# Kernel tuning notes

Measured on AMD Instinct MI355X. Metric: run time of the kernel, lower is better.

Reference implementation:

```python
import jax, jax.numpy as jnp
import numpy as np

N = 100000   # nodes
E = 1600000  # edges (avg degree 16)
D = 128      # in = hid = out dim
EPS = 1e-5   # BatchNorm eps


def setup_inputs() -> dict:
    key = jax.random.key(0)
    ks = jax.random.split(key, 14)
    x = jax.random.normal(ks[0], (N, D), dtype=jnp.float32)
    row = jax.random.randint(ks[1], (E,), 0, N, dtype=jnp.int32)
    col = jax.random.randint(ks[2], (E,), 0, N, dtype=jnp.int32)
    edge_weight = jax.random.uniform(ks[3], (E,), dtype=jnp.float32)
    s = 1.0 / np.sqrt(D)
    W0 = jax.random.uniform(ks[4], (D, D), jnp.float32, -s, s)
    b0 = jax.random.uniform(ks[5], (D,), jnp.float32, -s, s)
    W1 = jax.random.uniform(ks[6], (D, D), jnp.float32, -s, s)
    b1 = jax.random.uniform(ks[7], (D,), jnp.float32, -s, s)
    W2 = jax.random.uniform(ks[8], (D, D), jnp.float32, -s, s)
    b2 = jax.random.uniform(ks[9], (D,), jnp.float32, -s, s)
    g0 = jnp.ones((D,), jnp.float32); be0 = jnp.zeros((D,), jnp.float32)
    g1 = jnp.ones((D,), jnp.float32); be1 = jnp.zeros((D,), jnp.float32)
    return {"x": x, "edge_weight": edge_weight,
            "W0": W0, "b0": b0, "g0": g0, "be0": be0,
            "W1": W1, "b1": b1, "g1": g1, "be1": be1,
            "W2": W2, "b2": b2, "row": row, "col": col}


def _spmm(edge_weight, row, col, h):
    # (A_norm @ h) with A in COO: out[r] = sum_e w_e * h[col_e] for row_e == r
    return jax.ops.segment_sum(edge_weight[:, None] * h[col], row, num_segments=N)


def _bn(h, gamma, beta):
    # BatchNorm1d, training-mode stats (biased variance), over the node axis
    m = h.mean(axis=0)
    v = h.var(axis=0)
    return gamma * (h - m) * jax.lax.rsqrt(v + EPS) + beta


def reference(x, edge_weight, W0, b0, g0, be0, W1, b1, g1, be1, W2, b2, row, col):
    # hidden block 1: SpMM(A, Linear(h)) -> BN -> ReLU (dropout p=0)
    h = jax.nn.relu(_bn(_spmm(edge_weight, row, col, x @ W0 + b0), g0, be0))
    # hidden block 2
    h = jax.nn.relu(_bn(_spmm(edge_weight, row, col, h @ W1 + b1), g1, be1))
    # final layer: SpMM(A, Linear(h)), no BN/activation
    return _spmm(edge_weight, row, col, h @ W2 + b2)
```

## Files before the change

### kernel.cpp

```cpp
#include <hip/hip_runtime.h>
#include <cstddef>

#define DD 128
#define EPS 1e-5f

typedef short short8 __attribute__((ext_vector_type(8)));
typedef float float4v __attribute__((ext_vector_type(4)));

__device__ __forceinline__ unsigned short f2bf(float f) {
    union { float f; unsigned int u; } x; x.f = f;
    unsigned int r = x.u + 0x7fffu + ((x.u >> 16) & 1u);
    return (unsigned short)(r >> 16);
}
__device__ __forceinline__ float bfhi2f(unsigned int hi_bits) {
    union { unsigned int u; float f; } x; x.u = hi_bits;
    return x.f;
}


__global__ void hist_kernel(const int* __restrict__ row, int* __restrict__ deg, int E) {
    int e = blockIdx.x * blockDim.x + threadIdx.x;
    if (e < E) atomicAdd(&deg[row[e]], 1);
}

__global__ void scanA_kernel(const int* __restrict__ deg, int* __restrict__ tmp,
                             int* __restrict__ bsum, int n) {
    __shared__ int s[1024];
    int tid = threadIdx.x;
    int gid = blockIdx.x * 1024 + tid;
    int v = (gid < n) ? ((deg[gid] + 3) & ~3) : 0;
    s[tid] = v;
    __syncthreads();
    for (int off = 1; off < 1024; off <<= 1) {
        int t = s[tid];
        int u = (tid >= off) ? s[tid - off] : 0;
        __syncthreads();
        s[tid] = t + u;
        __syncthreads();
    }
    if (gid < n) tmp[gid] = s[tid];
    if (tid == 1023) bsum[blockIdx.x] = s[1023];
}

__global__ void scanB_kernel(const int* __restrict__ bsum, int* __restrict__ boff,
                             int* __restrict__ row_start, int nb, int n) {
    __shared__ int s[128];
    int tid = threadIdx.x;
    int v = (tid < nb) ? bsum[tid] : 0;
    s[tid] = v;
    __syncthreads();
    for (int off = 1; off < 128; off <<= 1) {
        int t = s[tid];
        int u = (tid >= off) ? s[tid - off] : 0;
        __syncthreads();
        s[tid] = t + u;
        __syncthreads();
    }
    if (tid < nb) boff[tid] = s[tid] - v;
    if (tid == nb - 1) row_start[n] = s[tid];
}

__global__ void scanC_kernel(const int* __restrict__ deg, const int* __restrict__ tmp,
                             const int* __restrict__ boff, int* __restrict__ row_start,
                             int* __restrict__ cursor, int n) {
    int gid = blockIdx.x * 1024 + threadIdx.x;
    if (gid < n) {
        int pd = (deg[gid] + 3) & ~3;
        int rs = tmp[gid] - pd + boff[blockIdx.x];
        row_start[gid] = rs;
        cursor[gid] = rs;
    }
}


__global__ void bcur_init_kernel(const int* __restrict__ row_start,
                                 int* __restrict__ bcur, int nb) {
    int b = blockIdx.x * 256 + threadIdx.x;
    if (b < nb) bcur[b] = row_start[b << 8];
}

__global__ __launch_bounds__(256) void scatter_phase1_kernel(
    const int* __restrict__ row, const int* __restrict__ col,
    const float* __restrict__ ew, int* __restrict__ bcur,
    unsigned long long* __restrict__ ebuf2, int E, int nbuck) {
    __shared__ int hist[512];
    __shared__ int cur[512];
    int tid = threadIdx.x;
    int b = blockIdx.x;
    int C = (E + gridDim.x - 1) / gridDim.x;
    int e0 = b * C, e1 = min(E, e0 + C);
    for (int t = tid; t < nbuck; t += 256) hist[t] = 0;
    __syncthreads();
    for (int e = e0 + tid; e < e1; e += 256)
        atomicAdd(&hist[row[e] >> 8], 1);
    __syncthreads();
    for (int i = tid; i < nbuck; i += 256) {
        int t = i + b * 37;
        t -= (t >= nbuck) ? nbuck * (t / nbuck) : 0;
        int h = hist[t];
        cur[t] = h ? atomicAdd(&bcur[t], h) : 0;
    }
    __syncthreads();
    for (int e = e0 + tid; e < e1; e += 256) {
        int r = row[e];
        int bk = r >> 8;
        int pos = atomicAdd(&cur[bk], 1);
        unsigned long long pk = (unsigned long long)((unsigned int)col[e]
                              | ((unsigned int)(r & 255) << 24))
                              | ((unsigned long long)__float_as_uint(ew[e]) << 32);
        ebuf2[pos] = pk;
    }
}

#define P2CAP 6144

__global__ __launch_bounds__(256) void scatter_phase2_kernel(
    const unsigned long long* __restrict__ ebuf2, const int* __restrict__ row_start,
    const int* __restrict__ bcur_final, int* __restrict__ cursor,
    unsigned long long* __restrict__ ebuf, int N) {
    __shared__ int cur[256];
    __shared__ unsigned long long outb[P2CAP];
    int b = blockIdx.x;
    int r_lo = b << 8;
    int r_hi = min(N, r_lo + 256);
    int e_lo = row_start[r_lo];
    int e_hi = row_start[r_hi];
    int cnt_pad = e_hi - e_lo;
    int cnt_real = bcur_final[b] - e_lo;
    int tid = threadIdx.x;
    if (cnt_pad <= P2CAP) {
        int r = r_lo + tid;
        cur[tid] = (r < N) ? (row_start[r] - e_lo) : 0;
        for (int i = tid; i < cnt_pad; i += 256) outb[i] = 0ull;
        __syncthreads();
        for (int i = e_lo + tid; i < e_lo + cnt_real; i += 256) {
            unsigned long long pk = ebuf2[i];
            int rl = (int)((unsigned int)(pk >> 24) & 255u);
            int pos = atomicAdd(&cur[rl], 1);
            outb[pos] = pk & 0xFFFFFFFF0001FFFFull;
        }
        __syncthreads();
        for (int i = tid; i < cnt_pad; i += 256)
            ebuf[e_lo + i] = outb[i];
    } else {
        for (int i = e_lo + tid; i < e_hi; i += 256) ebuf[i] = 0ull;
        __threadfence();
        __syncthreads();
        for (int i = e_lo + tid; i < e_lo + cnt_real; i += 256) {
            unsigned long long pk = ebuf2[i];
            int rl = (int)((unsigned int)(pk >> 24) & 255u);
            int pos = atomicAdd(&cursor[r_lo + rl], 1);
            ebuf[pos] = pk & 0xFFFFFFFF0001FFFFull;
        }
    }
}


__global__ void convw_kernel(const float* __restrict__ W0, const float* __restrict__ W1,
                             const float* __restrict__ W2, unsigned short* __restrict__ T0,
                             unsigned short* __restrict__ T1, unsigned short* __restrict__ T2) {
    const float* W = (blockIdx.y == 0) ? W0 : (blockIdx.y == 1) ? W1 : W2;
    unsigned short* T = (blockIdx.y == 0) ? T0 : (blockIdx.y == 1) ? T1 : T2;
    int gid = blockIdx.x * 256 + threadIdx.x;
    int k = gid >> 7, n = gid & 127;
    T[n * DD + k] = f2bf(W[k * DD + n]);
}


__global__ __launch_bounds__(256) void gemm_mfma_f32_kernel(
    const float* __restrict__ A, const unsigned short* __restrict__ Wt,
    const float* __restrict__ bias, unsigned short* __restrict__ H, int nrows)
{
    __shared__ unsigned short Asl[64][136];
    __shared__ unsigned short Wsl[128][136];

    const int tid  = threadIdx.x;
    const int row0 = blockIdx.x * 64;

    for (int i = tid; i < 2048; i += 256) {
        int r = i >> 4, off = (i & 15) * 8;
        *(uint4*)&Wsl[r][off] = *(const uint4*)(Wt + (size_t)r * DD + off);
    }
    for (int i = tid; i < 2048; i += 256) {
        int r = i >> 5, off4 = i & 31;
        int grow = row0 + r;
        float4 v = make_float4(0.f, 0.f, 0.f, 0.f);
        if (grow < nrows)
            v = *(const float4*)(A + (size_t)grow * DD + off4 * 4);
        ushort4 p;
        p.x = f2bf(v.x); p.y = f2bf(v.y); p.z = f2bf(v.z); p.w = f2bf(v.w);
        *(ushort4*)&Asl[r][off4 * 4] = p;
    }
    __syncthreads();

    const int w = tid >> 6, lane = tid & 63;
    const int m = lane & 15, q = lane >> 4;

    short8 afr[4];
    #pragma unroll
    for (int c = 0; c < 4; ++c)
        afr[c] = *(const short8*)&Asl[w * 16 + m][c * 32 + q * 8];

    float4v acc[8];
    #pragma unroll
    for (int t = 0; t < 8; ++t) acc[t] = (float4v){0.f, 0.f, 0.f, 0.f};

    #pragma unroll
    for (int t = 0; t < 8; ++t) {
        #pragma unroll
        for (int c = 0; c < 4; ++c) {
            short8 bfr = *(const short8*)&Wsl[t * 16 + m][c * 32 + q * 8];
            acc[t] = __builtin_amdgcn_mfma_f32_16x16x32_bf16(afr[c], bfr, acc[t], 0, 0, 0);
        }
    }

    #pragma unroll
    for (int t = 0; t < 8; ++t) {
        float bv = bias[t * 16 + m];
        #pragma unroll
        for (int i = 0; i < 4; ++i)
            Asl[w * 16 + q * 4 + i][t * 16 + m] = f2bf(acc[t][i] + bv);
    }
    __syncthreads();

    for (int i = tid; i < 1024; i += 256) {
        int r = i >> 4, off = (i & 15) * 8;
        if (row0 + r < nrows)
            *(uint4*)(H + (size_t)(row0 + r) * DD + off) = *(const uint4*)&Asl[r][off];
    }
}


__global__ __launch_bounds__(256) void gemm_mfma_bf16_kernel(
    const unsigned int* __restrict__ A, const unsigned short* __restrict__ Wt,
    const float* __restrict__ bias,
    const float* __restrict__ sums, const float* __restrict__ g,
    const float* __restrict__ be,
    unsigned short* __restrict__ H, int nrows)
{
    __shared__ unsigned short Asl[64][136];
    __shared__ unsigned short Wsl[128][136];
    __shared__ float scl_s[128], sft_s[128];

    const int tid  = threadIdx.x;
    const int row0 = blockIdx.x * 64;

    if (tid < 128) {
        float inv_n = 1.0f / (float)nrows;
        float mean = sums[tid] * inv_n;
        float var = sums[128 + tid] * inv_n - mean * mean;
        float rstd = rsqrtf(var + EPS);
        float sc = g[tid] * rstd;
        scl_s[tid] = sc;
        sft_s[tid] = be[tid] - mean * sc;
    }

    for (int i = tid; i < 2048; i += 256) {
        int r = i >> 4, off = (i & 15) * 8;
        *(uint4*)&Wsl[r][off] = *(const uint4*)(Wt + (size_t)r * DD + off);
    }
    __syncthreads();

    for (int i = tid; i < 1024; i += 256) {
        int r = i >> 4, ch = (i & 15) * 8;
        int grow = row0 + r;
        uint4 u = make_uint4(0, 0, 0, 0);
        if (grow < nrows)
            u = *(const uint4*)(A + (size_t)grow * 64 + (ch >> 1));
        unsigned int uu[4] = {u.x, u.y, u.z, u.w};
        unsigned int outp[4];
        #pragma unroll
        for (int j = 0; j < 4; ++j) {
            float vx = bfhi2f(uu[j] << 16);
            float vy = bfhi2f(uu[j] & 0xffff0000u);
            int k = ch + j * 2;
            vx = fmaxf(0.f, vx * scl_s[k] + sft_s[k]);
            vy = fmaxf(0.f, vy * scl_s[k + 1] + sft_s[k + 1]);
            outp[j] = (unsigned int)f2bf(vx) | ((unsigned int)f2bf(vy) << 16);
        }
        *(uint4*)&Asl[r][ch] = *(const uint4*)outp;
    }
    __syncthreads();

    const int w = tid >> 6, lane = tid & 63;
    const int m = lane & 15, q = lane >> 4;

    short8 afr[4];
    #pragma unroll
    for (int c = 0; c < 4; ++c)
        afr[c] = *(const short8*)&Asl[w * 16 + m][c * 32 + q * 8];

    float4v acc[8];
    #pragma unroll
    for (int t = 0; t < 8; ++t) acc[t] = (float4v){0.f, 0.f, 0.f, 0.f};

    #pragma unroll
    for (int t = 0; t < 8; ++t) {
        #pragma unroll
        for (int c = 0; c < 4; ++c) {
            short8 bfr = *(const short8*)&Wsl[t * 16 + m][c * 32 + q * 8];
            acc[t] = __builtin_amdgcn_mfma_f32_16x16x32_bf16(afr[c], bfr, acc[t], 0, 0, 0);
        }
    }

    #pragma unroll
    for (int t = 0; t < 8; ++t) {
        float bv = bias[t * 16 + m];
        #pragma unroll
        for (int i = 0; i < 4; ++i)
            Asl[w * 16 + q * 4 + i][t * 16 + m] = f2bf(acc[t][i] + bv);
    }
    __syncthreads();

    for (int i = tid; i < 1024; i += 256) {
        int r = i >> 4, off = (i & 15) * 8;
        if (row0 + r < nrows)
            *(uint4*)(H + (size_t)(row0 + r) * DD + off) = *(const uint4*)&Asl[r][off];
    }
}


__global__ __launch_bounds__(256, 8) void spmm_bf16_kernel(
    const unsigned short* __restrict__ H, const int* __restrict__ ps,
    const unsigned long long* __restrict__ ebuf,
    float* __restrict__ Sf, unsigned int* __restrict__ Sb, int writeBF,
    int N, int K)
{
    const int lane = threadIdx.x & 63;
    const int g = lane >> 4;
    const int p = lane & 15;
    const int wave = (blockIdx.x << 2) | (threadIdx.x >> 6);
    int r0 = wave * K;
    if (r0 >= N) return;
    int r1 = min(N, r0 + K);

    const unsigned short* Hp = H + p * 8;

    int r = r0;
    int e = ps[r0];
    const int eEnd = ps[r1];

    while (r < r1 && ps[r + 1] == e) {
        if (g == 0) {
            if (writeBF) {
                uint4 z = make_uint4(0, 0, 0, 0);
                *(uint4*)(Sb + (size_t)r * 64 + p * 4) = z;
            } else {
                float4 z = make_float4(0.f, 0.f, 0.f, 0.f);
                *(float4*)(Sf + (size_t)r * DD + p * 8) = z;
                *(float4*)(Sf + (size_t)r * DD + p * 8 + 4) = z;
            }
        }
        ++r;
    }
    if (r >= r1) return;
    int next_end = ps[r + 1];

    unsigned long long pk_cur = __builtin_nontemporal_load(&ebuf[e + g]);
    int i1 = e + 4; i1 = (i1 < eEnd) ? i1 : e;
    unsigned long long pk_nxt = __builtin_nontemporal_load(&ebuf[i1 + g]);
    uint4 u_cur = *(const uint4*)(Hp + (size_t)(unsigned int)pk_cur * DD);

    float acc[8];
    #pragma unroll
    for (int j = 0; j < 8; ++j) acc[j] = 0.f;

    for (; e < eEnd; e += 4) {
        int i2 = e + 8; i2 = (i2 < eEnd) ? i2 : e;
        unsigned long long pk_f = __builtin_nontemporal_load(&ebuf[i2 + g]);
        uint4 u_nxt = *(const uint4*)(Hp + (size_t)(unsigned int)pk_nxt * DD);
        float wj = __uint_as_float((unsigned int)(pk_cur >> 32));
        unsigned int uu[4] = {u_cur.x, u_cur.y, u_cur.z, u_cur.w};
        #pragma unroll
        for (int q4 = 0; q4 < 4; ++q4) {
            acc[2 * q4]     += wj * bfhi2f(uu[q4] << 16);
            acc[2 * q4 + 1] += wj * bfhi2f(uu[q4] & 0xffff0000u);
        }

        while (e + 4 == next_end) {
            #pragma unroll
            for (int j = 0; j < 8; ++j) {
                acc[j] += __shfl_xor(acc[j], 16);
                acc[j] += __shfl_xor(acc[j], 32);
            }
            if (g == 0) {
                if (writeBF) {
                    unsigned int o[4];
                    #pragma unroll
                    for (int j = 0; j < 4; ++j)
                        o[j] = (unsigned int)f2bf(acc[2 * j])
                             | ((unsigned int)f2bf(acc[2 * j + 1]) << 16);
                    *(uint4*)(Sb + (size_t)r * 64 + p * 4) = *(const uint4*)o;
                } else {
                    float4 lo = make_float4(acc[0], acc[1], acc[2], acc[3]);
                    float4 hi = make_float4(acc[4], acc[5], acc[6], acc[7]);
                    *(float4*)(Sf + (size_t)r * DD + p * 8) = lo;
                    *(float4*)(Sf + (size_t)r * DD + p * 8 + 4) = hi;
                }
            }
            #pragma unroll
            for (int j = 0; j < 8; ++j) acc[j] = 0.f;
            ++r;
            if (r >= r1) break;
            next_end = ps[r + 1];
        }

        pk_cur = pk_nxt;
        u_cur  = u_nxt;
        pk_nxt = pk_f;
    }
}


__global__ void bn_stats_bf16_kernel(const unsigned int* __restrict__ Sb,
                                     float* __restrict__ sums, int n) {
    __shared__ float lsx[256], lsx2[256], lsy[256], lsy2[256];
    int tid = threadIdx.x;
    int c2 = tid & 63;
    float sx = 0.f, sx2 = 0.f, sy = 0.f, sy2 = 0.f;
    int total = n * 64;
    for (int i = blockIdx.x * 256 + tid; i < total; i += 256 * 256) {
        unsigned int u = Sb[i];
        float vx = bfhi2f(u << 16);
        float vy = bfhi2f(u & 0xffff0000u);
        sx += vx; sx2 += vx * vx;
        sy += vy; sy2 += vy * vy;
    }
    lsx[tid] = sx; lsx2[tid] = sx2; lsy[tid] = sy; lsy2[tid] = sy2;
    __syncthreads();
    if (tid < 64) {
        sx  = lsx[tid]  + lsx[tid + 64]  + lsx[tid + 128]  + lsx[tid + 192];
        sx2 = lsx2[tid] + lsx2[tid + 64] + lsx2[tid + 128] + lsx2[tid + 192];
        sy  = lsy[tid]  + lsy[tid + 64]  + lsy[tid + 128]  + lsy[tid + 192];
        sy2 = lsy2[tid] + lsy2[tid + 64] + lsy2[tid + 128] + lsy2[tid + 192];
        atomicAdd(&sums[2 * c2], sx);
        atomicAdd(&sums[2 * c2 + 1], sy);
        atomicAdd(&sums[128 + 2 * c2], sx2);
        atomicAdd(&sums[129 + 2 * c2], sy2);
    }
}


extern "C" void kernel_launch(void* const* d_in, const int* in_sizes, int n_in,
                              void* d_out, int out_size, void* d_ws, size_t ws_size,
                              hipStream_t stream) {
    const float* x   = (const float*)d_in[0];
    const float* ew  = (const float*)d_in[1];
    const float* W0  = (const float*)d_in[2];
    const float* b0  = (const float*)d_in[3];
    const float* g0  = (const float*)d_in[4];
    const float* be0 = (const float*)d_in[5];
    const float* W1  = (const float*)d_in[6];
    const float* b1  = (const float*)d_in[7];
    const float* g1  = (const float*)d_in[8];
    const float* be1 = (const float*)d_in[9];
    const float* W2  = (const float*)d_in[10];
    const float* b2  = (const float*)d_in[11];
    const int* row   = (const int*)d_in[12];
    const int* col   = (const int*)d_in[13];

    const int N = in_sizes[0] / DD;
    const int E = in_sizes[1];
    float* out = (float*)d_out;

    const size_t EPADCAP = (size_t)E + 3 * (size_t)N + 64;

    char* w = (char*)d_ws;
    unsigned short* H   = (unsigned short*)w; w += (size_t)N * DD * 2;
    unsigned int* Sb    = (unsigned int*)w;   w += (size_t)N * 64 * 4;
    unsigned long long* ebuf = (unsigned long long*)w; w += EPADCAP * 8;
    unsigned short* Wt0 = (unsigned short*)w; w += DD * DD * 2;
    unsigned short* Wt1 = (unsigned short*)w; w += DD * DD * 2;
    unsigned short* Wt2 = (unsigned short*)w; w += DD * DD * 2;
    float* sums         = (float*)w;          w += 256 * 4;
    int*   deg          = (int*)w;            w += (size_t)N * 4;
    int*   tmp          = (int*)w;            w += (size_t)N * 4;
    int*   cursor       = (int*)w;            w += (size_t)N * 4;
    int*   bsum         = (int*)w;            w += 128 * 4;
    int*   boff         = (int*)w;            w += 128 * 4;
    int*   row_start    = (int*)w;            w += (size_t)(N + 1) * 4;

    unsigned long long* ebuf2 = (unsigned long long*)Sb;
    int* bcur = tmp;
    int nbuck = (N + 255) >> 8;

    hipMemsetAsync(deg, 0, (size_t)N * 4, stream);
    hist_kernel<<<(E + 255) / 256, 256, 0, stream>>>(row, deg, E);
    int NB = (N + 1023) / 1024;
    scanA_kernel<<<NB, 1024, 0, stream>>>(deg, tmp, bsum, N);
    scanB_kernel<<<1, 128, 0, stream>>>(bsum, boff, row_start, NB, N);
    scanC_kernel<<<NB, 1024, 0, stream>>>(deg, tmp, boff, row_start, cursor, N);
    bcur_init_kernel<<<(nbuck + 255) / 256, 256, 0, stream>>>(row_start, bcur, nbuck);
    scatter_phase1_kernel<<<256, 256, 0, stream>>>(row, col, ew, bcur, ebuf2, E, nbuck);
    scatter_phase2_kernel<<<nbuck, 256, 0, stream>>>(ebuf2, row_start, bcur, cursor, ebuf, N);

    convw_kernel<<<dim3(64, 3), 256, 0, stream>>>(W0, W1, W2, Wt0, Wt1, Wt2);

    int gblocks = (N + 63) / 64;

    const int SPMM_BLOCKS = 2048;
    const int totalWaves = SPMM_BLOCKS * 4;
    const int K = (N + totalWaves - 1) / totalWaves;

    gemm_mfma_f32_kernel<<<gblocks, 256, 0, stream>>>(x, Wt0, b0, H, N);
    spmm_bf16_kernel<<<SPMM_BLOCKS, 256, 0, stream>>>(H, row_start, ebuf, nullptr, Sb, 1, N, K);
    hipMemsetAsync(sums, 0, 256 * 4, stream);
    bn_stats_bf16_kernel<<<256, 256, 0, stream>>>(Sb, sums, N);

    gemm_mfma_bf16_kernel<<<gblocks, 256, 0, stream>>>(Sb, Wt1, b1, sums, g0, be0, H, N);
    spmm_bf16_kernel<<<SPMM_BLOCKS, 256, 0, stream>>>(H, row_start, ebuf, nullptr, Sb, 1, N, K);
    hipMemsetAsync(sums, 0, 256 * 4, stream);
    bn_stats_bf16_kernel<<<256, 256, 0, stream>>>(Sb, sums, N);

    gemm_mfma_bf16_kernel<<<gblocks, 256, 0, stream>>>(Sb, Wt2, b2, sums, g1, be1, H, N);
    spmm_bf16_kernel<<<SPMM_BLOCKS, 256, 0, stream>>>(H, row_start, ebuf, out, nullptr, 0, N, K);
}
```

Baseline: 583.6 us.

## Fuse BN statistics into SpMM epilogue and load GEMM A-fragments directly from global

The separate BN-stats kernel is removed. Each SpMM wave now accumulates per-channel sums and squared sums of the bf16 outputs it writes and reduces them per block into a partial buffer, and a small reduce kernel atomically combines those partials. This avoids re-reading the full hidden activation from memory twice per forward pass. The GEMM kernels skip staging A in LDS and load and convert their MFMA A-fragments straight from global memory. The bcur init kernel is folded into scanC, and the SpMM grid is doubled to 4096 blocks. The trade-offs are added LDS, syncthreads and registers in the SpMM kernel, and a new partial buffer of SPMM_BLOCKS*256 floats in the workspace.

```diff
diff --git a/kernel.cpp b/kernel.cpp
--- a/kernel.cpp
+++ b/kernel.cpp
@@ -62,22 +62,17 @@
 
 __global__ void scanC_kernel(const int* __restrict__ deg, const int* __restrict__ tmp,
                              const int* __restrict__ boff, int* __restrict__ row_start,
-                             int* __restrict__ cursor, int n) {
+                             int* __restrict__ cursor, int* __restrict__ bcur, int n) {
     int gid = blockIdx.x * 1024 + threadIdx.x;
     if (gid < n) {
         int pd = (deg[gid] + 3) & ~3;
         int rs = tmp[gid] - pd + boff[blockIdx.x];
         row_start[gid] = rs;
         cursor[gid] = rs;
-    }
-}
-
-
-__global__ void bcur_init_kernel(const int* __restrict__ row_start,
-                                 int* __restrict__ bcur, int nb) {
-    int b = blockIdx.x * 256 + threadIdx.x;
-    if (b < nb) bcur[b] = row_start[b << 8];
-}
+        if ((gid & 255) == 0) bcur[gid >> 8] = rs;
+    }
+}
+
 
 __global__ __launch_bounds__(256) void scatter_phase1_kernel(
     const int* __restrict__ row, const int* __restrict__ col,
@@ -181,25 +176,29 @@
         int r = i >> 4, off = (i & 15) * 8;
         *(uint4*)&Wsl[r][off] = *(const uint4*)(Wt + (size_t)r * DD + off);
     }
-    for (int i = tid; i < 2048; i += 256) {
-        int r = i >> 5, off4 = i & 31;
-        int grow = row0 + r;
-        float4 v = make_float4(0.f, 0.f, 0.f, 0.f);
-        if (grow < nrows)
-            v = *(const float4*)(A + (size_t)grow * DD + off4 * 4);
-        ushort4 p;
-        p.x = f2bf(v.x); p.y = f2bf(v.y); p.z = f2bf(v.z); p.w = f2bf(v.w);
-        *(ushort4*)&Asl[r][off4 * 4] = p;
-    }
     __syncthreads();
 
     const int w = tid >> 6, lane = tid & 63;
     const int m = lane & 15, q = lane >> 4;
+    const int grow = row0 + w * 16 + m;
+    const bool inb = grow < nrows;
 
     short8 afr[4];
     #pragma unroll
-    for (int c = 0; c < 4; ++c)
-        afr[c] = *(const short8*)&Asl[w * 16 + m][c * 32 + q * 8];
+    for (int c = 0; c < 4; ++c) {
+        float4 v0 = make_float4(0.f, 0.f, 0.f, 0.f);
+        float4 v1 = v0;
+        if (inb) {
+            v0 = *(const float4*)(A + (size_t)grow * DD + c * 32 + q * 8);
+            v1 = *(const float4*)(A + (size_t)grow * DD + c * 32 + q * 8 + 4);
+        }
+        short8 t;
+        t[0] = (short)f2bf(v0.x); t[1] = (short)f2bf(v0.y);
+        t[2] = (short)f2bf(v0.z); t[3] = (short)f2bf(v0.w);
+        t[4] = (short)f2bf(v1.x); t[5] = (short)f2bf(v1.y);
+        t[6] = (short)f2bf(v1.z); t[7] = (short)f2bf(v1.w);
+        afr[c] = t;
+    }
 
     float4v acc[8];
     #pragma unroll
@@ -261,34 +260,29 @@
     }
     __syncthreads();
 
-    for (int i = tid; i < 1024; i += 256) {
-        int r = i >> 4, ch = (i & 15) * 8;
-        int grow = row0 + r;
-        uint4 u = make_uint4(0, 0, 0, 0);
-        if (grow < nrows)
-            u = *(const uint4*)(A + (size_t)grow * 64 + (ch >> 1));
-        unsigned int uu[4] = {u.x, u.y, u.z, u.w};
-        unsigned int outp[4];
+    const int w = tid >> 6, lane = tid & 63;
+    const int m = lane & 15, q = lane >> 4;
+    const int grow = row0 + w * 16 + m;
+    const bool inb = grow < nrows;
+
+    short8 afr[4];
+    #pragma unroll
+    for (int c = 0; c < 4; ++c) {
+        uint4 ua = make_uint4(0, 0, 0, 0);
+        if (inb)
+            ua = *(const uint4*)(A + (size_t)grow * 64 + c * 16 + q * 4);
+        unsigned int uu[4] = {ua.x, ua.y, ua.z, ua.w};
+        short8 t;
         #pragma unroll
         for (int j = 0; j < 4; ++j) {
-            float vx = bfhi2f(uu[j] << 16);
-            float vy = bfhi2f(uu[j] & 0xffff0000u);
-            int k = ch + j * 2;
-            vx = fmaxf(0.f, vx * scl_s[k] + sft_s[k]);
-            vy = fmaxf(0.f, vy * scl_s[k + 1] + sft_s[k + 1]);
-            outp[j] = (unsigned int)f2bf(vx) | ((unsigned int)f2bf(vy) << 16);
-        }
-        *(uint4*)&Asl[r][ch] = *(const uint4*)outp;
-    }
-    __syncthreads();
-
-    const int w = tid >> 6, lane = tid & 63;
-    const int m = lane & 15, q = lane >> 4;
-
-    short8 afr[4];
-    #pragma unroll
-    for (int c = 0; c < 4; ++c)
-        afr[c] = *(const short8*)&Asl[w * 16 + m][c * 32 + q * 8];
+            int k = c * 32 + q * 8 + 2 * j;
+            float vx = fmaxf(0.f, bfhi2f(uu[j] << 16) * scl_s[k] + sft_s[k]);
+            float vy = fmaxf(0.f, bfhi2f(uu[j] & 0xffff0000u) * scl_s[k + 1] + sft_s[k + 1]);
+            t[2 * j]     = (short)f2bf(vx);
+            t[2 * j + 1] = (short)f2bf(vy);
+        }
+        afr[c] = t;
+    }
 
     float4v acc[8];
     #pragma unroll
@@ -324,120 +318,141 @@
     const unsigned short* __restrict__ H, const int* __restrict__ ps,
     const unsigned long long* __restrict__ ebuf,
     float* __restrict__ Sf, unsigned int* __restrict__ Sb, int writeBF,
-    int N, int K)
+    float* __restrict__ pbuf, int N, int K)
 {
-    const int lane = threadIdx.x & 63;
+    __shared__ float sred[1024];
+
+    const int tid  = threadIdx.x;
+    const int lane = tid & 63;
     const int g = lane >> 4;
     const int p = lane & 15;
-    const int wave = (blockIdx.x << 2) | (threadIdx.x >> 6);
-    int r0 = wave * K;
-    if (r0 >= N) return;
-    int r1 = min(N, r0 + K);
-
-    const unsigned short* Hp = H + p * 8;
-
-    int r = r0;
-    int e = ps[r0];
-    const int eEnd = ps[r1];
-
-    while (r < r1 && ps[r + 1] == e) {
-        if (g == 0) {
-            if (writeBF) {
-                uint4 z = make_uint4(0, 0, 0, 0);
-                *(uint4*)(Sb + (size_t)r * 64 + p * 4) = z;
-            } else {
-                float4 z = make_float4(0.f, 0.f, 0.f, 0.f);
-                *(float4*)(Sf + (size_t)r * DD + p * 8) = z;
-                *(float4*)(Sf + (size_t)r * DD + p * 8 + 4) = z;
-            }
-        }
-        ++r;
-    }
-    if (r >= r1) return;
-    int next_end = ps[r + 1];
-
-    unsigned long long pk_cur = __builtin_nontemporal_load(&ebuf[e + g]);
-    int i1 = e + 4; i1 = (i1 < eEnd) ? i1 : e;
-    unsigned long long pk_nxt = __builtin_nontemporal_load(&ebuf[i1 + g]);
-    uint4 u_cur = *(const uint4*)(Hp + (size_t)(unsigned int)pk_cur * DD);
-
-    float acc[8];
-    #pragma unroll
-    for (int j = 0; j < 8; ++j) acc[j] = 0.f;
-
-    for (; e < eEnd; e += 4) {
-        int i2 = e + 8; i2 = (i2 < eEnd) ? i2 : e;
-        unsigned long long pk_f = __builtin_nontemporal_load(&ebuf[i2 + g]);
-        uint4 u_nxt = *(const uint4*)(Hp + (size_t)(unsigned int)pk_nxt * DD);
-        float wj = __uint_as_float((unsigned int)(pk_cur >> 32));
-        unsigned int uu[4] = {u_cur.x, u_cur.y, u_cur.z, u_cur.w};
-        #pragma unroll
-        for (int q4 = 0; q4 < 4; ++q4) {
-            acc[2 * q4]     += wj * bfhi2f(uu[q4] << 16);
-            acc[2 * q4 + 1] += wj * bfhi2f(uu[q4] & 0xffff0000u);
-        }
-
-        while (e + 4 == next_end) {
-            #pragma unroll
-            for (int j = 0; j < 8; ++j) {
-                acc[j] += __shfl_xor(acc[j], 16);
-                acc[j] += __shfl_xor(acc[j], 32);
-            }
+    const int wv = tid >> 6;
+    const int wave = (blockIdx.x << 2) | wv;
+    const int r0 = wave * K;
+    const bool active = (r0 < N);
+
+    float st_s[8], st_q[8];
+    #pragma unroll
+    for (int j = 0; j < 8; ++j) { st_s[j] = 0.f; st_q[j] = 0.f; }
+
+    if (active) {
+        const int r1 = min(N, r0 + K);
+        const unsigned short* Hp = H + p * 8;
+
+        int r = r0;
+        int e = ps[r0];
+        const int eEnd = ps[r1];
+
+        while (r < r1 && ps[r + 1] == e) {
             if (g == 0) {
                 if (writeBF) {
-                    unsigned int o[4];
-                    #pragma unroll
-                    for (int j = 0; j < 4; ++j)
-                        o[j] = (unsigned int)f2bf(acc[2 * j])
-                             | ((unsigned int)f2bf(acc[2 * j + 1]) << 16);
-                    *(uint4*)(Sb + (size_t)r * 64 + p * 4) = *(const uint4*)o;
+                    uint4 z = make_uint4(0, 0, 0, 0);
+                    *(uint4*)(Sb + (size_t)r * 64 + p * 4) = z;
                 } else {
-                    float4 lo = make_float4(acc[0], acc[1], acc[2], acc[3]);
-                    float4 hi = make_float4(acc[4], acc[5], acc[6], acc[7]);
-                    *(float4*)(Sf + (size_t)r * DD + p * 8) = lo;
-                    *(float4*)(Sf + (size_t)r * DD + p * 8 + 4) = hi;
+                    float4 z = make_float4(0.f, 0.f, 0.f, 0.f);
+                    *(float4*)(Sf + (size_t)r * DD + p * 8) = z;
+                    *(float4*)(Sf + (size_t)r * DD + p * 8 + 4) = z;
                 }
             }
+            ++r;
+        }
+
+        if (r < r1) {
+            int next_end = ps[r + 1];
+
+            unsigned long long pk_cur = __builtin_nontemporal_load(&ebuf[e + g]);
+            int i1 = e + 4; i1 = (i1 < eEnd) ? i1 : e;
+            unsigned long long pk_nxt = __builtin_nontemporal_load(&ebuf[i1 + g]);
+            uint4 u_cur = *(const uint4*)(Hp + (size_t)(unsigned int)pk_cur * DD);
+
+            float acc[8];
             #pragma unroll
             for (int j = 0; j < 8; ++j) acc[j] = 0.f;
-            ++r;
-            if (r >= r1) break;
-            next_end = ps[r + 1];
-        }
-
-        pk_cur = pk_nxt;
-        u_cur  = u_nxt;
-        pk_nxt = pk_f;
-    }
-}
-
-
-__global__ void bn_stats_bf16_kernel(const unsigned int* __restrict__ Sb,
-                                     float* __restrict__ sums, int n) {
-    __shared__ float lsx[256], lsx2[256], lsy[256], lsy2[256];
-    int tid = threadIdx.x;
-    int c2 = tid & 63;
-    float sx = 0.f, sx2 = 0.f, sy = 0.f, sy2 = 0.f;
-    int total = n * 64;
-    for (int i = blockIdx.x * 256 + tid; i < total; i += 256 * 256) {
-        unsigned int u = Sb[i];
-        float vx = bfhi2f(u << 16);
-        float vy = bfhi2f(u & 0xffff0000u);
-        sx += vx; sx2 += vx * vx;
-        sy += vy; sy2 += vy * vy;
-    }
-    lsx[tid] = sx; lsx2[tid] = sx2; lsy[tid] = sy; lsy2[tid] = sy2;
-    __syncthreads();
-    if (tid < 64) {
-        sx  = lsx[tid]  + lsx[tid + 64]  + lsx[tid + 128]  + lsx[tid + 192];
-        sx2 = lsx2[tid] + lsx2[tid + 64] + lsx2[tid + 128] + lsx2[tid + 192];
-        sy  = lsy[tid]  + lsy[tid + 64]  + lsy[tid + 128]  + lsy[tid + 192];
-        sy2 = lsy2[tid] + lsy2[tid + 64] + lsy2[tid + 128] + lsy2[tid + 192];
-        atomicAdd(&sums[2 * c2], sx);
-        atomicAdd(&sums[2 * c2 + 1], sy);
-        atomicAdd(&sums[128 + 2 * c2], sx2);
-        atomicAdd(&sums[129 + 2 * c2], sy2);
-    }
+
+            for (; e < eEnd; e += 4) {
+                int i2 = e + 8; i2 = (i2 < eEnd) ? i2 : e;
+                unsigned long long pk_f = __builtin_nontemporal_load(&ebuf[i2 + g]);
+                uint4 u_nxt = *(const uint4*)(Hp + (size_t)(unsigned int)pk_nxt * DD);
+                float wj = __uint_as_float((unsigned int)(pk_cur >> 32));
+                unsigned int uu[4] = {u_cur.x, u_cur.y, u_cur.z, u_cur.w};
+                #pragma unroll
+                for (int q4 = 0; q4 < 4; ++q4) {
+                    acc[2 * q4]     += wj * bfhi2f(uu[q4] << 16);
+                    acc[2 * q4 + 1] += wj * bfhi2f(uu[q4] & 0xffff0000u);
+                }
+
+                while (e + 4 == next_end) {
+                    #pragma unroll
+                    for (int j = 0; j < 8; ++j) {
+                        acc[j] += __shfl_xor(acc[j], 16);
+                        acc[j] += __shfl_xor(acc[j], 32);
+                    }
+                    if (g == 0) {
+                        if (writeBF) {
+                            unsigned int o[4];
+                            #pragma unroll
+                            for (int j = 0; j < 4; ++j)
+                                o[j] = (unsigned int)f2bf(acc[2 * j])
+                                     | ((unsigned int)f2bf(acc[2 * j + 1]) << 16);
+                            *(uint4*)(Sb + (size_t)r * 64 + p * 4) = *(const uint4*)o;
+                            if (pbuf) {
+                                #pragma unroll
+                                for (int j = 0; j < 4; ++j) {
+                                    float vx = bfhi2f(o[j] << 16);
+                                    float vy = bfhi2f(o[j] & 0xffff0000u);
+                                    st_s[2 * j] += vx; st_q[2 * j] += vx * vx;
+                                    st_s[2 * j + 1] += vy; st_q[2 * j + 1] += vy * vy;
+                                }
+                            }
+                        } else {
+                            float4 lo = make_float4(acc[0], acc[1], acc[2], acc[3]);
+                            float4 hi = make_float4(acc[4], acc[5], acc[6], acc[7]);
+                            *(float4*)(Sf + (size_t)r * DD + p * 8) = lo;
+                            *(float4*)(Sf + (size_t)r * DD + p * 8 + 4) = hi;
+                        }
+                    }
+                    #pragma unroll
+                    for (int j = 0; j < 8; ++j) acc[j] = 0.f;
+                    ++r;
+                    if (r >= r1) break;
+                    next_end = ps[r + 1];
+                }
+
+                pk_cur = pk_nxt;
+                u_cur  = u_nxt;
+                pk_nxt = pk_f;
+            }
+        }
+    }
+
+    if (pbuf) {
+        for (int i = tid; i < 1024; i += 256) sred[i] = 0.f;
+        __syncthreads();
+        if (active && g == 0) {
+            #pragma unroll
+            for (int k = 0; k < 8; ++k) {
+                sred[wv * 128 + p * 8 + k]       = st_s[k];
+                sred[512 + wv * 128 + p * 8 + k] = st_q[k];
+            }
+        }
+        __syncthreads();
+        {
+            int part = tid >> 7, ch = tid & 127;
+            int base = part * 512 + ch;
+            float v = sred[base] + sred[base + 128] + sred[base + 256] + sred[base + 384];
+            pbuf[(size_t)blockIdx.x * 256 + tid] = v;
+        }
+    }
+}
+
+
+__global__ __launch_bounds__(256) void bn_reduce_kernel(
+    const float* __restrict__ pbuf, float* __restrict__ sums, int nb) {
+    int c = threadIdx.x;
+    float s = 0.f;
+    for (int b = blockIdx.x; b < nb; b += gridDim.x)
+        s += pbuf[(size_t)b * 256 + c];
+    atomicAdd(&sums[c], s);
 }
 
 
@@ -463,12 +478,15 @@
     const int E = in_sizes[1];
     float* out = (float*)d_out;
 
+    const int SPMM_BLOCKS = 4096;
+
     const size_t EPADCAP = (size_t)E + 3 * (size_t)N + 64;
 
     char* w = (char*)d_ws;
     unsigned short* H   = (unsigned short*)w; w += (size_t)N * DD * 2;
     unsigned int* Sb    = (unsigned int*)w;   w += (size_t)N * 64 * 4;
     unsigned long long* ebuf = (unsigned long long*)w; w += EPADCAP * 8;
+    float* pbuf         = (float*)w;          w += (size_t)SPMM_BLOCKS * 256 * 4;
     unsigned short* Wt0 = (unsigned short*)w; w += DD * DD * 2;
     unsigned short* Wt1 = (unsigned short*)w; w += DD * DD * 2;
     unsigned short* Wt2 = (unsigned short*)w; w += DD * DD * 2;
@@ -489,8 +507,7 @@
     int NB = (N + 1023) / 1024;
     scanA_kernel<<<NB, 1024, 0, stream>>>(deg, tmp, bsum, N);
     scanB_kernel<<<1, 128, 0, stream>>>(bsum, boff, row_start, NB, N);
-    scanC_kernel<<<NB, 1024, 0, stream>>>(deg, tmp, boff, row_start, cursor, N);
-    bcur_init_kernel<<<(nbuck + 255) / 256, 256, 0, stream>>>(row_start, bcur, nbuck);
+    scanC_kernel<<<NB, 1024, 0, stream>>>(deg, tmp, boff, row_start, cursor, bcur, N);
     scatter_phase1_kernel<<<256, 256, 0, stream>>>(row, col, ew, bcur, ebuf2, E, nbuck);
     scatter_phase2_kernel<<<nbuck, 256, 0, stream>>>(ebuf2, row_start, bcur, cursor, ebuf, N);
 
@@ -498,20 +515,19 @@
 
     int gblocks = (N + 63) / 64;
 
-    const int SPMM_BLOCKS = 2048;
     const int totalWaves = SPMM_BLOCKS * 4;
     const int K = (N + totalWaves - 1) / totalWaves;
 
     gemm_mfma_f32_kernel<<<gblocks, 256, 0, stream>>>(x, Wt0, b0, H, N);
-    spmm_bf16_kernel<<<SPMM_BLOCKS, 256, 0, stream>>>(H, row_start, ebuf, nullptr, Sb, 1, N, K);
     hipMemsetAsync(sums, 0, 256 * 4, stream);
-    bn_stats_bf16_kernel<<<256, 256, 0, stream>>>(Sb, sums, N);
+    spmm_bf16_kernel<<<SPMM_BLOCKS, 256, 0, stream>>>(H, row_start, ebuf, nullptr, Sb, 1, pbuf, N, K);
+    bn_reduce_kernel<<<64, 256, 0, stream>>>(pbuf, sums, SPMM_BLOCKS);
 
     gemm_mfma_bf16_kernel<<<gblocks, 256, 0, stream>>>(Sb, Wt1, b1, sums, g0, be0, H, N);
-    spmm_bf16_kernel<<<SPMM_BLOCKS, 256, 0, stream>>>(H, row_start, ebuf, nullptr, Sb, 1, N, K);
     hipMemsetAsync(sums, 0, 256 * 4, stream);
-    bn_stats_bf16_kernel<<<256, 256, 0, stream>>>(Sb, sums, N);
+    spmm_bf16_kernel<<<SPMM_BLOCKS, 256, 0, stream>>>(H, row_start, ebuf, nullptr, Sb, 1, pbuf, N, K);
+    bn_reduce_kernel<<<64, 256, 0, stream>>>(pbuf, sums, SPMM_BLOCKS);
 
     gemm_mfma_bf16_kernel<<<gblocks, 256, 0, stream>>>(Sb, Wt2, b2, sums, g1, be1, H, N);
-    spmm_bf16_kernel<<<SPMM_BLOCKS, 256, 0, stream>>>(H, row_start, ebuf, out, nullptr, 0, N, K);
-}
+    spmm_bf16_kernel<<<SPMM_BLOCKS, 256, 0, stream>>>(H, row_start, ebuf, out, nullptr, 0, nullptr, N, K);
+}
```

Measured after the change: 589.1 us. Within noise of the previous version (+1.0%).
